# Kernel tuning notes

Hardware: AMD Instinct MI355X
Metric: run time of the kernel (lower is better)

The kernel has to match this reference:

```python
import jax, jax.numpy as jnp
import numpy as np

DIM = 256
FFN_DIM = 512
NH = 8
EPS = 1e-5


def ln(x, g, b):
    m = x.mean(-1, keepdims=True)
    v = ((x - m) ** 2).mean(-1, keepdims=True)
    return (x - m) / jnp.sqrt(v + EPS) * g + b


def setup_inputs() -> dict:
    key = jax.random.key(0)
    ks = jax.random.split(key, 16)
    B, L, C, H, W = 16, 16384, DIM, 128, 128
    s = 0.02
    return {
        "query": jax.random.normal(ks[0], (B, 1, C), jnp.float32),
        "mem": jax.random.normal(ks[1], (B, L, C), jnp.float32),
        "ior_emb": jax.random.uniform(ks[2], (B, NH, H, W), jnp.float32),
        # input_proj: Linear(dim,dim) + ReLU + LayerNorm
        "W_ip": jax.random.normal(ks[3], (C, C), jnp.float32) * s,
        "b_ip": jnp.zeros((C,), jnp.float32),
        "g_ip": jnp.ones((C,), jnp.float32),
        "be_ip": jnp.zeros((C,), jnp.float32),
        # q / kv projections
        "W_q": jax.random.normal(ks[4], (C, C), jnp.float32) * s,
        "b_q": jnp.zeros((C,), jnp.float32),
        "W_kv": jax.random.normal(ks[5], (C, 2 * C), jnp.float32) * s,
        "b_kv": jnp.zeros((2 * C,), jnp.float32),
        # norm_q, norm_ffn
        "g_q": jnp.ones((C,), jnp.float32),
        "be_q": jnp.zeros((C,), jnp.float32),
        "g_f": jnp.ones((C,), jnp.float32),
        "be_f": jnp.zeros((C,), jnp.float32),
        # ffn (Mlp)
        "W1": jax.random.normal(ks[6], (C, FFN_DIM), jnp.float32) * s,
        "b1": jnp.zeros((FFN_DIM,), jnp.float32),
        "W2": jax.random.normal(ks[7], (FFN_DIM, C), jnp.float32) * s,
        "b2": jnp.zeros((C,), jnp.float32),
    }


def reference(query, mem, ior_emb, W_ip, b_ip, g_ip, be_ip, W_q, b_q, W_kv, b_kv,
              g_q, be_q, g_f, be_f, W1, b1, W2, b2):
    B, L, C = mem.shape
    nh = ior_emb.shape[1]
    hd = C // nh
    scale = hd ** -0.5
    # input_proj(mem): Linear -> ReLU -> LayerNorm
    m = ln(jax.nn.relu(mem @ W_ip + b_ip), g_ip, be_ip)  # [B,L,C]
    kv = m @ W_kv + b_kv
    k, v = kv[..., :C], kv[..., C:]
    q = ln(query, g_q, be_q) @ W_q + b_q  # [B,1,C]
    # per-head split along channel == reshape (..., nh, hd)
    qh = q.reshape(B, 1, nh, hd)
    kh = k.reshape(B, L, nh, hd)
    vh = v.reshape(B, L, nh, hd)
    ior = ior_emb.reshape(B, nh, 1, L)
    scores = jnp.einsum('bqhd,blhd->bhql', qh, kh) * scale * ior  # [B,nh,1,L]
    attn = jax.nn.softmax(scores, axis=-1)
    out = jnp.einsum('bhql,blhd->bqhd', attn, vh).reshape(B, 1, C)
    x = out + query
    h = ln(x, g_f, be_f)
    ffn = jax.nn.gelu(h @ W1 + b1, approximate=False) @ W2 + b2
    return x + ffn
```

## Files before the change

kernel.cpp:

```cpp
#include <hip/hip_runtime.h>
#include <math.h>

#define CDIM 256
#define LDIM 16384
#define NH 8
#define HD 32
#define FFN 512
#define EPS 1e-5f
#define SCALE 0.17677669529663687f

#define RB 64
#define CHUNKS (LDIM/RB)
#define LDA 264

typedef __attribute__((ext_vector_type(8))) short short8;
typedef __attribute__((ext_vector_type(4))) float f32x4;

__device__ inline unsigned short f2bf(float x) {
    unsigned int u = __float_as_uint(x);
    unsigned int lsb = (u >> 16) & 1u;
    u += 0x7fffu + lsb;
    return (unsigned short)(u >> 16);
}


__global__ __launch_bounds__(256) void convert_weights(const float* __restrict__ Wip,
                                                       const float* __restrict__ Wkv,
                                                       unsigned short* __restrict__ w1,
                                                       unsigned short* __restrict__ wkv) {
    int idx = blockIdx.x * 256 + threadIdx.x;
    if (idx < 65536) {
        int j = idx & 7, l = (idx >> 3) & 63, c = (idx >> 9) & 15, t = idx >> 13;
        int k = t * 32 + (l >> 4) * 8 + j;
        int col = c * 16 + (l & 15);
        w1[idx] = f2bf(Wip[k * CDIM + col]);
    }
    if (idx < 131072) {
        int j = idx & 7, l = (idx >> 3) & 63, c = (idx >> 9) & 31, t = idx >> 14;
        int k = t * 32 + (l >> 4) * 8 + j;
        int col = c * 16 + (l & 15);
        wkv[idx] = f2bf(Wkv[k * 2 * CDIM + col]);
    }
}


__global__ __launch_bounds__(256) void qprep_kernel(const float* __restrict__ query,
                                                    const float* __restrict__ Wq,
                                                    const float* __restrict__ bq,
                                                    const float* __restrict__ gq,
                                                    const float* __restrict__ beq,
                                                    float* __restrict__ qs) {
    int b = blockIdx.x;
    int tid = threadIdx.x;
    int wave = tid >> 6, lane = tid & 63;
    __shared__ float sh[CDIM];
    __shared__ float red[8];

    float x = query[b * CDIM + tid];
    float s = x, sq = x * x;
#pragma unroll
    for (int m = 32; m >= 1; m >>= 1) { s += __shfl_xor(s, m, 64); sq += __shfl_xor(sq, m, 64); }
    if (lane == 0) { red[wave] = s; red[4 + wave] = sq; }
    __syncthreads();
    float ts = red[0] + red[1] + red[2] + red[3];
    float tq = red[4] + red[5] + red[6] + red[7];
    float mean = ts * (1.f / CDIM);
    float var = tq * (1.f / CDIM) - mean * mean;
    float rstd = rsqrtf(var + EPS);
    sh[tid] = (x - mean) * rstd * gq[tid] + beq[tid];
    __syncthreads();

    float acc = bq[tid];
    for (int k = 0; k < CDIM; ++k) acc = fmaf(sh[k], Wq[k * CDIM + tid], acc);
    qs[b * CDIM + tid] = acc * SCALE;
}


__device__ inline void mfma_gemm(const unsigned short* __restrict__ smA,
                                 const unsigned short* __restrict__ wsw, int NC, int ctile0,
                                 int lx, int quad, f32x4 acc[4][4]) {
#pragma unroll
    for (int rt = 0; rt < 4; ++rt)
#pragma unroll
        for (int ci = 0; ci < 4; ++ci) acc[rt][ci] = (f32x4){0.f, 0.f, 0.f, 0.f};

    int l = quad * 16 + lx;
#pragma unroll
    for (int t = 0; t < 8; ++t) {
        short8 bfrag[4];
#pragma unroll
        for (int ci = 0; ci < 4; ++ci)
            bfrag[ci] = *(const short8*)(wsw + (((size_t)(t * NC + ctile0 + ci)) * 64 + l) * 8);
        short8 afrag[4];
#pragma unroll
        for (int rt = 0; rt < 4; ++rt)
            afrag[rt] = *(const short8*)(smA + (rt * 16 + lx) * LDA + t * 32 + quad * 8);
#pragma unroll
        for (int rt = 0; rt < 4; ++rt)
#pragma unroll
            for (int ci = 0; ci < 4; ++ci)
                acc[rt][ci] = __builtin_amdgcn_mfma_f32_16x16x32_bf16(afrag[rt], bfrag[ci], acc[rt][ci], 0, 0, 0);
    }
}


__global__ __launch_bounds__(256, 2) void main_kernel(const float* __restrict__ mem,
                                                      const unsigned short* __restrict__ w1,
                                                      const unsigned short* __restrict__ wkv,
                                                      const float* __restrict__ bip,
                                                      const float* __restrict__ gip,
                                                      const float* __restrict__ beip,
                                                      const float* __restrict__ bkv,
                                                      const float* __restrict__ ior,
                                                      const float* __restrict__ qs,
                                                      float* __restrict__ partials) {
    int blk = blockIdx.x;
    int b = blk / CHUNKS;
    int chunk = blk % CHUNKS;
    int row0 = chunk * RB;
    int tid = threadIdx.x;
    int w = tid >> 6, l = tid & 63;
    int quad = l >> 4, lx = l & 15;

    __shared__ unsigned short bufA[RB * LDA];
    __shared__ float iorS[NH][RB];
    __shared__ float redS[4][RB];
    __shared__ float redQ[4][RB];
    __shared__ float stats[2][RB];

    {
        int i0 = tid, i1 = tid + 256;
        int h0 = i0 >> 6, r0 = i0 & 63;
        int h1 = i1 >> 6, r1 = i1 & 63;
        iorS[h0][r0] = ior[((size_t)(b * NH + h0)) * LDIM + row0 + r0];
        iorS[h1][r1] = ior[((size_t)(b * NH + h1)) * LDIM + row0 + r1];
    }
    {
        const float4* src = (const float4*)(mem + ((size_t)b * LDIM + row0) * CDIM);
#pragma unroll
        for (int it = 0; it < 16; ++it) {
            int i = tid + 256 * it;
            int r = i >> 6, c4 = i & 63;
            float4 v = src[i];
            ushort4 u;
            u.x = f2bf(v.x); u.y = f2bf(v.y); u.z = f2bf(v.z); u.w = f2bf(v.w);
            *(ushort4*)&bufA[r * LDA + c4 * 4] = u;
        }
    }
    __syncthreads();

    int col[4];
#pragma unroll
    for (int ci = 0; ci < 4; ++ci) col[ci] = (4 * w + ci) * 16 + lx;

    f32x4 acc[4][4];
    mfma_gemm(bufA, w1, 16, 4 * w, lx, quad, acc);

    float bb[4], gg[4], ee[4];
#pragma unroll
    for (int ci = 0; ci < 4; ++ci) { bb[ci] = bip[col[ci]]; gg[ci] = gip[col[ci]]; ee[ci] = beip[col[ci]]; }

#pragma unroll
    for (int rt = 0; rt < 4; ++rt) {
#pragma unroll
        for (int reg = 0; reg < 4; ++reg) {
#pragma unroll
            for (int ci = 0; ci < 4; ++ci)
                acc[rt][ci][reg] = fmaxf(acc[rt][ci][reg] + bb[ci], 0.f);
            float s = acc[rt][0][reg] + acc[rt][1][reg] + acc[rt][2][reg] + acc[rt][3][reg];
            float q = acc[rt][0][reg] * acc[rt][0][reg] + acc[rt][1][reg] * acc[rt][1][reg]
                    + acc[rt][2][reg] * acc[rt][2][reg] + acc[rt][3][reg] * acc[rt][3][reg];
#pragma unroll
            for (int m = 8; m >= 1; m >>= 1) { s += __shfl_xor(s, m, 64); q += __shfl_xor(q, m, 64); }
            if (lx == 0) {
                int row = rt * 16 + quad * 4 + reg;
                redS[w][row] = s;
                redQ[w][row] = q;
            }
        }
    }
    __syncthreads();
    if (tid < RB) {
        float s = redS[0][tid] + redS[1][tid] + redS[2][tid] + redS[3][tid];
        float q = redQ[0][tid] + redQ[1][tid] + redQ[2][tid] + redQ[3][tid];
        float mean = s * (1.f / CDIM);
        float var = q * (1.f / CDIM) - mean * mean;
        stats[0][tid] = mean;
        stats[1][tid] = rsqrtf(var + EPS);
    }
    __syncthreads();

#pragma unroll
    for (int rt = 0; rt < 4; ++rt)
#pragma unroll
        for (int reg = 0; reg < 4; ++reg) {
            int row = rt * 16 + quad * 4 + reg;
            float mean = stats[0][row], rstd = stats[1][row];
#pragma unroll
            for (int ci = 0; ci < 4; ++ci) {
                float y = (acc[rt][ci][reg] - mean) * rstd * gg[ci] + ee[ci];
                bufA[row * LDA + col[ci]] = f2bf(y);
            }
        }
    __syncthreads();

    f32x4 acc2[4][4];
    mfma_gemm(bufA, wkv, 32, 4 * w, lx, quad, acc2);

    float qv[4], bk[4];
#pragma unroll
    for (int ci = 0; ci < 4; ++ci) { qv[ci] = qs[b * CDIM + col[ci]]; bk[ci] = bkv[col[ci]]; }

    float p0[16], p1[16];
    float M0 = -1e30f, M1 = -1e30f;
#pragma unroll
    for (int rt = 0; rt < 4; ++rt)
#pragma unroll
        for (int reg = 0; reg < 4; ++reg) {
            float s0 = (acc2[rt][0][reg] + bk[0]) * qv[0] + (acc2[rt][1][reg] + bk[1]) * qv[1];
            float s1 = (acc2[rt][2][reg] + bk[2]) * qv[2] + (acc2[rt][3][reg] + bk[3]) * qv[3];
#pragma unroll
            for (int m = 8; m >= 1; m >>= 1) { s0 += __shfl_xor(s0, m, 64); s1 += __shfl_xor(s1, m, 64); }
            int row = rt * 16 + quad * 4 + reg;
            s0 *= iorS[2 * w][row];
            s1 *= iorS[2 * w + 1][row];
            p0[rt * 4 + reg] = s0;
            p1[rt * 4 + reg] = s1;
            M0 = fmaxf(M0, s0);
            M1 = fmaxf(M1, s1);
        }
    M0 = fmaxf(M0, __shfl_xor(M0, 16, 64)); M0 = fmaxf(M0, __shfl_xor(M0, 32, 64));
    M1 = fmaxf(M1, __shfl_xor(M1, 16, 64)); M1 = fmaxf(M1, __shfl_xor(M1, 32, 64));
    float S0 = 0.f, S1 = 0.f;
#pragma unroll
    for (int i = 0; i < 16; ++i) {
        p0[i] = __expf(p0[i] - M0); S0 += p0[i];
        p1[i] = __expf(p1[i] - M1); S1 += p1[i];
    }
    S0 += __shfl_xor(S0, 16, 64); S0 += __shfl_xor(S0, 32, 64);
    S1 += __shfl_xor(S1, 16, 64); S1 += __shfl_xor(S1, 32, 64);

    f32x4 acc3[4][4];
    mfma_gemm(bufA, wkv, 32, 16 + 4 * w, lx, quad, acc3);

    float o[4];
#pragma unroll
    for (int ci = 0; ci < 4; ++ci) {
        float bo = bkv[CDIM + col[ci]];
        const float* pp = (ci < 2) ? p0 : p1;
        float a = 0.f;
#pragma unroll
        for (int rt = 0; rt < 4; ++rt)
#pragma unroll
            for (int reg = 0; reg < 4; ++reg)
                a = fmaf(pp[rt * 4 + reg], acc3[rt][ci][reg] + bo, a);
        a += __shfl_xor(a, 16, 64);
        a += __shfl_xor(a, 32, 64);
        o[ci] = a;
    }

    float* P0 = &partials[((size_t)blk * NH + 2 * w) * 34];
    float* P1 = P0 + 34;
    if (quad == 0) {
        P0[2 + lx] = o[0];
        P0[2 + 16 + lx] = o[1];
        P1[2 + lx] = o[2];
        P1[2 + 16 + lx] = o[3];
        if (lx == 0) { P0[0] = M0; P0[1] = S0; P1[0] = M1; P1[1] = S1; }
    }
}


__global__ __launch_bounds__(64) void combine_kernel(const float* __restrict__ partials,
                                                     float* __restrict__ attnout) {
    int bh = blockIdx.x;
    int b = bh >> 3, h = bh & 7;
    int lane = threadIdx.x;

    float M = -1e30f;
    for (int c = lane; c < CHUNKS; c += 64)
        M = fmaxf(M, partials[(((size_t)b * CHUNKS + c) * NH + h) * 34]);
#pragma unroll
    for (int m = 32; m >= 1; m >>= 1) M = fmaxf(M, __shfl_xor(M, m, 64));

    float S = 0.f;
    for (int c = lane; c < CHUNKS; c += 64) {
        const float* P = &partials[(((size_t)b * CHUNKS + c) * NH + h) * 34];
        S += P[1] * __expf(P[0] - M);
    }
#pragma unroll
    for (int m = 32; m >= 1; m >>= 1) S += __shfl_xor(S, m, 64);

    int d = lane & 31, half = lane >> 5;
    float O = 0.f;
    for (int c = half; c < CHUNKS; c += 2) {
        const float* P = &partials[(((size_t)b * CHUNKS + c) * NH + h) * 34];
        O = fmaf(P[2 + d], __expf(P[0] - M), O);
    }
    O += __shfl_xor(O, 32, 64);
    if (lane < 32) attnout[b * CDIM + h * HD + d] = O / S;
}


__global__ __launch_bounds__(256) void epilogue_kernel(const float* __restrict__ attnout,
                                                       const float* __restrict__ query,
                                                       const float* __restrict__ gf,
                                                       const float* __restrict__ bef,
                                                       const float* __restrict__ W1,
                                                       const float* __restrict__ b1,
                                                       const float* __restrict__ W2,
                                                       const float* __restrict__ b2,
                                                       float* __restrict__ out) {
    int b = blockIdx.x;
    int tid = threadIdx.x;
    int wave = tid >> 6, lane = tid & 63;
    __shared__ float sh[FFN];
    __shared__ float red[8];

    float x = attnout[b * CDIM + tid] + query[b * CDIM + tid];
    float s = x, sq = x * x;
#pragma unroll
    for (int m = 32; m >= 1; m >>= 1) { s += __shfl_xor(s, m, 64); sq += __shfl_xor(sq, m, 64); }
    if (lane == 0) { red[wave] = s; red[4 + wave] = sq; }
    __syncthreads();
    float ts = red[0] + red[1] + red[2] + red[3];
    float tq = red[4] + red[5] + red[6] + red[7];
    float mean = ts * (1.f / CDIM);
    float var = tq * (1.f / CDIM) - mean * mean;
    float rstd = rsqrtf(var + EPS);
    sh[tid] = (x - mean) * rstd * gf[tid] + bef[tid];
    __syncthreads();

    float t[2];
#pragma unroll
    for (int i = 0; i < 2; ++i) {
        int f = tid + 256 * i;
        float a = b1[f];
        for (int k = 0; k < CDIM; ++k) a = fmaf(sh[k], W1[k * FFN + f], a);
        t[i] = 0.5f * a * (1.f + erff(a * 0.7071067811865476f));
    }
    __syncthreads();
    sh[tid] = t[0];
    sh[tid + 256] = t[1];
    __syncthreads();

    float y = b2[tid];
    for (int f = 0; f < FFN; ++f) y = fmaf(sh[f], W2[f * CDIM + tid], y);
    out[b * CDIM + tid] = x + y;
}


extern "C" void kernel_launch(void* const* d_in, const int* in_sizes, int n_in,
                              void* d_out, int out_size, void* d_ws, size_t ws_size,
                              hipStream_t stream) {
    const float* query = (const float*)d_in[0];
    const float* mem   = (const float*)d_in[1];
    const float* ior   = (const float*)d_in[2];
    const float* Wip   = (const float*)d_in[3];
    const float* bip   = (const float*)d_in[4];
    const float* gip   = (const float*)d_in[5];
    const float* beip  = (const float*)d_in[6];
    const float* Wq    = (const float*)d_in[7];
    const float* bq    = (const float*)d_in[8];
    const float* Wkv   = (const float*)d_in[9];
    const float* bkv   = (const float*)d_in[10];
    const float* gq    = (const float*)d_in[11];
    const float* beq   = (const float*)d_in[12];
    const float* gf    = (const float*)d_in[13];
    const float* bef   = (const float*)d_in[14];
    const float* W1    = (const float*)d_in[15];
    const float* b1    = (const float*)d_in[16];
    const float* W2    = (const float*)d_in[17];
    const float* b2    = (const float*)d_in[18];
    float* out = (float*)d_out;

    char* ws = (char*)d_ws;
    float* qs             = (float*)(ws);
    float* attnout        = (float*)(ws + 16384);
    float* partials       = (float*)(ws + 32768);
    unsigned short* w1sw  = (unsigned short*)(ws + 32768 + 4456448);
    unsigned short* wkvsw = (unsigned short*)(ws + 32768 + 4456448 + 131072);

    const int B = 16;

    convert_weights<<<512, 256, 0, stream>>>(Wip, Wkv, w1sw, wkvsw);
    qprep_kernel<<<B, 256, 0, stream>>>(query, Wq, bq, gq, beq, qs);
    main_kernel<<<B * CHUNKS, 256, 0, stream>>>(mem, w1sw, wkvsw, bip, gip, beip, bkv, ior, qs, partials);
    combine_kernel<<<B * NH, 64, 0, stream>>>(partials, attnout);
    epilogue_kernel<<<B, 256, 0, stream>>>(attnout, query, gf, bef, W1, b1, W2, b2, out);
}
```

Before: 612.8 us.

## Fold K and V projections into query-side and post-softmax matmuls

```diff
diff --git a/kernel.cpp b/kernel.cpp
--- a/kernel.cpp
+++ b/kernel.cpp
@@ -10,11 +10,14 @@
 #define SCALE 0.17677669529663687f
 
 #define RB 64
-#define CHUNKS (LDIM/RB)
+#define NCHUNK 256
 #define LDA 264
+#define PSTRIDE 258
 
 typedef __attribute__((ext_vector_type(8))) short short8;
 typedef __attribute__((ext_vector_type(4))) float f32x4;
+
+union U8 { short8 s8; unsigned u[4]; };
 
 __device__ inline unsigned short f2bf(float x) {
     unsigned int u = __float_as_uint(x);
@@ -25,22 +28,12 @@
 
 
 __global__ __launch_bounds__(256) void convert_weights(const float* __restrict__ Wip,
-                                                       const float* __restrict__ Wkv,
-                                                       unsigned short* __restrict__ w1,
-                                                       unsigned short* __restrict__ wkv) {
+                                                       unsigned short* __restrict__ w1) {
     int idx = blockIdx.x * 256 + threadIdx.x;
-    if (idx < 65536) {
-        int j = idx & 7, l = (idx >> 3) & 63, c = (idx >> 9) & 15, t = idx >> 13;
-        int k = t * 32 + (l >> 4) * 8 + j;
-        int col = c * 16 + (l & 15);
-        w1[idx] = f2bf(Wip[k * CDIM + col]);
-    }
-    if (idx < 131072) {
-        int j = idx & 7, l = (idx >> 3) & 63, c = (idx >> 9) & 31, t = idx >> 14;
-        int k = t * 32 + (l >> 4) * 8 + j;
-        int col = c * 16 + (l & 15);
-        wkv[idx] = f2bf(Wkv[k * 2 * CDIM + col]);
-    }
+    int j = idx & 7, l = (idx >> 3) & 63, c = (idx >> 9) & 15, t = idx >> 13;
+    int k = t * 32 + (l >> 4) * 8 + j;
+    int colc = c * 16 + (l & 15);
+    w1[idx] = f2bf(Wip[k * CDIM + colc]);
 }
 
 
@@ -49,11 +42,16 @@
                                                     const float* __restrict__ bq,
                                                     const float* __restrict__ gq,
                                                     const float* __restrict__ beq,
-                                                    float* __restrict__ qs) {
+                                                    const float* __restrict__ Wkv,
+                                                    const float* __restrict__ bkv,
+                                                    float* __restrict__ qs,
+                                                    unsigned short* __restrict__ wts,
+                                                    float* __restrict__ qcb) {
     int b = blockIdx.x;
     int tid = threadIdx.x;
     int wave = tid >> 6, lane = tid & 63;
     __shared__ float sh[CDIM];
+    __shared__ float qsh[CDIM];
     __shared__ float red[8];
 
     float x = query[b * CDIM + tid];
@@ -72,7 +70,34 @@
 
     float acc = bq[tid];
     for (int k = 0; k < CDIM; ++k) acc = fmaf(sh[k], Wq[k * CDIM + tid], acc);
-    qs[b * CDIM + tid] = acc * SCALE;
+    float qv = acc * SCALE;
+    qs[b * CDIM + tid] = qv;
+    qsh[tid] = qv;
+    __syncthreads();
+
+    float wa[8];
+#pragma unroll
+    for (int h = 0; h < 8; ++h) wa[h] = 0.f;
+    const float* wr = Wkv + (size_t)tid * (2 * CDIM);
+#pragma unroll
+    for (int h = 0; h < 8; ++h)
+#pragma unroll
+        for (int d = 0; d < 32; ++d)
+            wa[h] = fmaf(wr[h * 32 + d], qsh[h * 32 + d], wa[h]);
+    unsigned short* wb = wts + (b << 12) + ((tid >> 5) << 9) + (((tid >> 3) & 3) << 7) + (tid & 7);
+#pragma unroll
+    for (int h = 0; h < 8; ++h) wb[h << 3] = f2bf(wa[h]);
+#pragma unroll
+    for (int h = 8; h < 16; ++h) wb[h << 3] = 0;
+
+    if (tid < 16) {
+        float cb = 0.f;
+        if (tid < 8) {
+#pragma unroll
+            for (int d = 0; d < 32; ++d) cb = fmaf(bkv[tid * 32 + d], qsh[tid * 32 + d], cb);
+        }
+        qcb[b * 16 + tid] = cb;
+    }
 }
 
 
@@ -104,36 +129,53 @@
 }
 
 
-__global__ __launch_bounds__(256, 2) void main_kernel(const float* __restrict__ mem,
+__device__ inline void mfma_svec(const unsigned short* __restrict__ smA,
+                                 const unsigned short* __restrict__ wt,
+                                 int lx, int quad, f32x4 accS[4]) {
+#pragma unroll
+    for (int rt = 0; rt < 4; ++rt) accS[rt] = (f32x4){0.f, 0.f, 0.f, 0.f};
+    int l = quad * 16 + lx;
+#pragma unroll
+    for (int t = 0; t < 8; ++t) {
+        short8 bf = *(const short8*)(wt + ((t * 64 + l) << 3));
+        short8 af[4];
+#pragma unroll
+        for (int rt = 0; rt < 4; ++rt)
+            af[rt] = *(const short8*)(smA + (rt * 16 + lx) * LDA + t * 32 + quad * 8);
+#pragma unroll
+        for (int rt = 0; rt < 4; ++rt)
+            accS[rt] = __builtin_amdgcn_mfma_f32_16x16x32_bf16(af[rt], bf, accS[rt], 0, 0, 0);
+    }
+}
+
+
+__global__ __launch_bounds__(256, 4) void main_kernel(const float* __restrict__ mem,
                                                       const unsigned short* __restrict__ w1,
-                                                      const unsigned short* __restrict__ wkv,
+                                                      const unsigned short* __restrict__ wts,
                                                       const float* __restrict__ bip,
                                                       const float* __restrict__ gip,
                                                       const float* __restrict__ beip,
-                                                      const float* __restrict__ bkv,
+                                                      const float* __restrict__ qcb,
                                                       const float* __restrict__ ior,
-                                                      const float* __restrict__ qs,
                                                       float* __restrict__ partials) {
     int blk = blockIdx.x;
-    int b = blk / CHUNKS;
-    int chunk = blk % CHUNKS;
+    int b = blk >> 8;
+    int chunk = blk & 255;
     int row0 = chunk * RB;
     int tid = threadIdx.x;
-    int w = tid >> 6, l = tid & 63;
-    int quad = l >> 4, lx = l & 15;
+    int w = tid >> 6, lane = tid & 63;
+    int quad = lane >> 4, lx = lane & 15;
 
     __shared__ unsigned short bufA[RB * LDA];
-    __shared__ float iorS[NH][RB];
+    __shared__ float iorS[NH][66];
     __shared__ float redS[4][RB];
     __shared__ float redQ[4][RB];
     __shared__ float stats[2][RB];
 
     {
         int i0 = tid, i1 = tid + 256;
-        int h0 = i0 >> 6, r0 = i0 & 63;
-        int h1 = i1 >> 6, r1 = i1 & 63;
-        iorS[h0][r0] = ior[((size_t)(b * NH + h0)) * LDIM + row0 + r0];
-        iorS[h1][r1] = ior[((size_t)(b * NH + h1)) * LDIM + row0 + r1];
+        iorS[i0 >> 6][i0 & 63] = ior[((size_t)(b * NH + (i0 >> 6))) * LDIM + row0 + (i0 & 63)];
+        iorS[i1 >> 6][i1 & 63] = ior[((size_t)(b * NH + (i1 >> 6))) * LDIM + row0 + (i1 & 63)];
     }
     {
         const float4* src = (const float4*)(mem + ((size_t)b * LDIM + row0) * CDIM);
@@ -167,138 +209,182 @@
 #pragma unroll
             for (int ci = 0; ci < 4; ++ci)
                 acc[rt][ci][reg] = fmaxf(acc[rt][ci][reg] + bb[ci], 0.f);
-            float s = acc[rt][0][reg] + acc[rt][1][reg] + acc[rt][2][reg] + acc[rt][3][reg];
-            float q = acc[rt][0][reg] * acc[rt][0][reg] + acc[rt][1][reg] * acc[rt][1][reg]
-                    + acc[rt][2][reg] * acc[rt][2][reg] + acc[rt][3][reg] * acc[rt][3][reg];
-#pragma unroll
-            for (int m = 8; m >= 1; m >>= 1) { s += __shfl_xor(s, m, 64); q += __shfl_xor(q, m, 64); }
+            float s2 = acc[rt][0][reg] + acc[rt][1][reg] + acc[rt][2][reg] + acc[rt][3][reg];
+            float q2 = acc[rt][0][reg] * acc[rt][0][reg] + acc[rt][1][reg] * acc[rt][1][reg]
+                     + acc[rt][2][reg] * acc[rt][2][reg] + acc[rt][3][reg] * acc[rt][3][reg];
+#pragma unroll
+            for (int m = 8; m >= 1; m >>= 1) { s2 += __shfl_xor(s2, m, 64); q2 += __shfl_xor(q2, m, 64); }
             if (lx == 0) {
                 int row = rt * 16 + quad * 4 + reg;
-                redS[w][row] = s;
-                redQ[w][row] = q;
+                redS[w][row] = s2;
+                redQ[w][row] = q2;
             }
         }
     }
     __syncthreads();
     if (tid < RB) {
-        float s = redS[0][tid] + redS[1][tid] + redS[2][tid] + redS[3][tid];
-        float q = redQ[0][tid] + redQ[1][tid] + redQ[2][tid] + redQ[3][tid];
-        float mean = s * (1.f / CDIM);
-        float var = q * (1.f / CDIM) - mean * mean;
+        float s2 = redS[0][tid] + redS[1][tid] + redS[2][tid] + redS[3][tid];
+        float q2 = redQ[0][tid] + redQ[1][tid] + redQ[2][tid] + redQ[3][tid];
+        float mean = s2 * (1.f / CDIM);
+        float var = q2 * (1.f / CDIM) - mean * mean;
         stats[0][tid] = mean;
         stats[1][tid] = rsqrtf(var + EPS);
     }
     __syncthreads();
 
-#pragma unroll
-    for (int rt = 0; rt < 4; ++rt)
+    unsigned ypk0[4][4], ypk1[4][4];
+#pragma unroll
+    for (int rt = 0; rt < 4; ++rt) {
+        float mn[4], rs[4];
 #pragma unroll
         for (int reg = 0; reg < 4; ++reg) {
             int row = rt * 16 + quad * 4 + reg;
-            float mean = stats[0][row], rstd = stats[1][row];
-#pragma unroll
-            for (int ci = 0; ci < 4; ++ci) {
-                float y = (acc[rt][ci][reg] - mean) * rstd * gg[ci] + ee[ci];
-                bufA[row * LDA + col[ci]] = f2bf(y);
-            }
-        }
-    __syncthreads();
-
-    f32x4 acc2[4][4];
-    mfma_gemm(bufA, wkv, 32, 4 * w, lx, quad, acc2);
-
-    float qv[4], bk[4];
-#pragma unroll
-    for (int ci = 0; ci < 4; ++ci) { qv[ci] = qs[b * CDIM + col[ci]]; bk[ci] = bkv[col[ci]]; }
-
-    float p0[16], p1[16];
-    float M0 = -1e30f, M1 = -1e30f;
+            mn[reg] = stats[0][row];
+            rs[reg] = stats[1][row];
+        }
+#pragma unroll
+        for (int ci = 0; ci < 4; ++ci) {
+            unsigned short u0 = f2bf((acc[rt][ci][0] - mn[0]) * rs[0] * gg[ci] + ee[ci]);
+            unsigned short u1 = f2bf((acc[rt][ci][1] - mn[1]) * rs[1] * gg[ci] + ee[ci]);
+            unsigned short u2 = f2bf((acc[rt][ci][2] - mn[2]) * rs[2] * gg[ci] + ee[ci]);
+            unsigned short u3 = f2bf((acc[rt][ci][3] - mn[3]) * rs[3] * gg[ci] + ee[ci]);
+            int rbase = rt * 16 + quad * 4;
+            bufA[(rbase + 0) * LDA + col[ci]] = u0;
+            bufA[(rbase + 1) * LDA + col[ci]] = u1;
+            bufA[(rbase + 2) * LDA + col[ci]] = u2;
+            bufA[(rbase + 3) * LDA + col[ci]] = u3;
+            ypk0[rt][ci] = (unsigned)u0 | ((unsigned)u1 << 16);
+            ypk1[rt][ci] = (unsigned)u2 | ((unsigned)u3 << 16);
+        }
+    }
+    __syncthreads();
+
+    f32x4 accS[4];
+    mfma_svec(bufA, wts + ((size_t)b << 12), lx, quad, accS);
+
+    float qcv = qcb[(b << 4) + lx];
+    float p[16];
+    float cmax = -1e30f;
 #pragma unroll
     for (int rt = 0; rt < 4; ++rt)
 #pragma unroll
         for (int reg = 0; reg < 4; ++reg) {
-            float s0 = (acc2[rt][0][reg] + bk[0]) * qv[0] + (acc2[rt][1][reg] + bk[1]) * qv[1];
-            float s1 = (acc2[rt][2][reg] + bk[2]) * qv[2] + (acc2[rt][3][reg] + bk[3]) * qv[3];
-#pragma unroll
-            for (int m = 8; m >= 1; m >>= 1) { s0 += __shfl_xor(s0, m, 64); s1 += __shfl_xor(s1, m, 64); }
             int row = rt * 16 + quad * 4 + reg;
-            s0 *= iorS[2 * w][row];
-            s1 *= iorS[2 * w + 1][row];
-            p0[rt * 4 + reg] = s0;
-            p1[rt * 4 + reg] = s1;
-            M0 = fmaxf(M0, s0);
-            M1 = fmaxf(M1, s1);
-        }
-    M0 = fmaxf(M0, __shfl_xor(M0, 16, 64)); M0 = fmaxf(M0, __shfl_xor(M0, 32, 64));
-    M1 = fmaxf(M1, __shfl_xor(M1, 16, 64)); M1 = fmaxf(M1, __shfl_xor(M1, 32, 64));
-    float S0 = 0.f, S1 = 0.f;
-#pragma unroll
-    for (int i = 0; i < 16; ++i) {
-        p0[i] = __expf(p0[i] - M0); S0 += p0[i];
-        p1[i] = __expf(p1[i] - M1); S1 += p1[i];
-    }
-    S0 += __shfl_xor(S0, 16, 64); S0 += __shfl_xor(S0, 32, 64);
-    S1 += __shfl_xor(S1, 16, 64); S1 += __shfl_xor(S1, 32, 64);
-
-    f32x4 acc3[4][4];
-    mfma_gemm(bufA, wkv, 32, 16 + 4 * w, lx, quad, acc3);
-
-    float o[4];
-#pragma unroll
-    for (int ci = 0; ci < 4; ++ci) {
-        float bo = bkv[CDIM + col[ci]];
-        const float* pp = (ci < 2) ? p0 : p1;
-        float a = 0.f;
-#pragma unroll
-        for (int rt = 0; rt < 4; ++rt)
-#pragma unroll
-            for (int reg = 0; reg < 4; ++reg)
-                a = fmaf(pp[rt * 4 + reg], acc3[rt][ci][reg] + bo, a);
-        a += __shfl_xor(a, 16, 64);
-        a += __shfl_xor(a, 32, 64);
-        o[ci] = a;
-    }
-
-    float* P0 = &partials[((size_t)blk * NH + 2 * w) * 34];
-    float* P1 = P0 + 34;
-    if (quad == 0) {
-        P0[2 + lx] = o[0];
-        P0[2 + 16 + lx] = o[1];
-        P1[2 + lx] = o[2];
-        P1[2 + 16 + lx] = o[3];
-        if (lx == 0) { P0[0] = M0; P0[1] = S0; P1[0] = M1; P1[1] = S1; }
-    }
-}
-
-
-__global__ __launch_bounds__(64) void combine_kernel(const float* __restrict__ partials,
-                                                     float* __restrict__ attnout) {
+            float sc = (accS[rt][reg] + qcv) * iorS[lx & 7][row];
+            p[rt * 4 + reg] = sc;
+            cmax = fmaxf(cmax, sc);
+        }
+    cmax = fmaxf(cmax, __shfl_xor(cmax, 16, 64));
+    cmax = fmaxf(cmax, __shfl_xor(cmax, 32, 64));
+    float csum = 0.f;
+#pragma unroll
+    for (int i = 0; i < 16; ++i) { p[i] = __expf(p[i] - cmax); csum += p[i]; }
+    csum += __shfl_xor(csum, 16, 64);
+    csum += __shfl_xor(csum, 32, 64);
+
+    f32x4 accPV[4];
+#pragma unroll
+    for (int ci = 0; ci < 4; ++ci) accPV[ci] = (f32x4){0.f, 0.f, 0.f, 0.f};
+
+    int srcA = ((quad & 1) << 5) + lx;
+    int srcB = srcA + 16;
+    bool hiQ = quad >= 2;
+#pragma unroll
+    for (int t2 = 0; t2 < 2; ++t2) {
+        float pe[8];
+#pragma unroll
+        for (int jj = 0; jj < 4; ++jj) {
+            float v0 = __shfl(p[t2 * 8 + jj], srcA, 64);
+            float v1 = __shfl(p[t2 * 8 + 4 + jj], srcA, 64);
+            pe[jj] = hiQ ? v1 : v0;
+            float v2 = __shfl(p[t2 * 8 + jj], srcB, 64);
+            float v3 = __shfl(p[t2 * 8 + 4 + jj], srcB, 64);
+            pe[4 + jj] = hiQ ? v3 : v2;
+        }
+        U8 pa;
+        pa.u[0] = (unsigned)f2bf(pe[0]) | ((unsigned)f2bf(pe[1]) << 16);
+        pa.u[1] = (unsigned)f2bf(pe[2]) | ((unsigned)f2bf(pe[3]) << 16);
+        pa.u[2] = (unsigned)f2bf(pe[4]) | ((unsigned)f2bf(pe[5]) << 16);
+        pa.u[3] = (unsigned)f2bf(pe[6]) | ((unsigned)f2bf(pe[7]) << 16);
+
+#pragma unroll
+        for (int ci = 0; ci < 4; ++ci) {
+            unsigned a0 = (unsigned)__shfl((int)ypk0[t2 * 2][ci], srcA, 64);
+            unsigned b0 = (unsigned)__shfl((int)ypk0[t2 * 2 + 1][ci], srcA, 64);
+            unsigned a1 = (unsigned)__shfl((int)ypk1[t2 * 2][ci], srcA, 64);
+            unsigned b1 = (unsigned)__shfl((int)ypk1[t2 * 2 + 1][ci], srcA, 64);
+            unsigned a2 = (unsigned)__shfl((int)ypk0[t2 * 2][ci], srcB, 64);
+            unsigned b2 = (unsigned)__shfl((int)ypk0[t2 * 2 + 1][ci], srcB, 64);
+            unsigned a3 = (unsigned)__shfl((int)ypk1[t2 * 2][ci], srcB, 64);
+            unsigned b3 = (unsigned)__shfl((int)ypk1[t2 * 2 + 1][ci], srcB, 64);
+            U8 ub;
+            ub.u[0] = hiQ ? b0 : a0;
+            ub.u[1] = hiQ ? b1 : a1;
+            ub.u[2] = hiQ ? b2 : a2;
+            ub.u[3] = hiQ ? b3 : a3;
+            accPV[ci] = __builtin_amdgcn_mfma_f32_16x16x32_bf16(pa.s8, ub.s8, accPV[ci], 0, 0, 0);
+        }
+    }
+
+    size_t pb = ((size_t)(b * NCHUNK + chunk)) * NH * PSTRIDE;
+    if (quad < 2) {
+#pragma unroll
+        for (int reg = 0; reg < 4; ++reg) {
+            float* dst = partials + pb + (size_t)(quad * 4 + reg) * PSTRIDE;
+#pragma unroll
+            for (int ci = 0; ci < 4; ++ci) dst[col[ci]] = accPV[ci][reg];
+        }
+    }
+    if (quad == 0 && lx < 8) {
+        float* dst = partials + pb + (size_t)lx * PSTRIDE;
+        dst[256] = cmax;
+        dst[257] = csum;
+    }
+}
+
+
+__global__ __launch_bounds__(256) void combine_kernel(const float* __restrict__ partials,
+                                                      const float* __restrict__ Wkv,
+                                                      const float* __restrict__ bkv,
+                                                      float* __restrict__ attnout) {
     int bh = blockIdx.x;
     int b = bh >> 3, h = bh & 7;
-    int lane = threadIdx.x;
-
+    int tid = threadIdx.x;
+    __shared__ float ms[NCHUNK], wf[NCHUNK], mt[CDIM];
+    __shared__ float sredA[4];
+    __shared__ float ored[8][33];
+
+    const float* base = partials + ((size_t)b * NCHUNK * NH + h) * PSTRIDE;
+    ms[tid] = base[(size_t)tid * NH * PSTRIDE + 256];
+    __syncthreads();
     float M = -1e30f;
-    for (int c = lane; c < CHUNKS; c += 64)
-        M = fmaxf(M, partials[(((size_t)b * CHUNKS + c) * NH + h) * 34]);
-#pragma unroll
-    for (int m = 32; m >= 1; m >>= 1) M = fmaxf(M, __shfl_xor(M, m, 64));
-
-    float S = 0.f;
-    for (int c = lane; c < CHUNKS; c += 64) {
-        const float* P = &partials[(((size_t)b * CHUNKS + c) * NH + h) * 34];
-        S += P[1] * __expf(P[0] - M);
-    }
-#pragma unroll
-    for (int m = 32; m >= 1; m >>= 1) S += __shfl_xor(S, m, 64);
-
-    int d = lane & 31, half = lane >> 5;
-    float O = 0.f;
-    for (int c = half; c < CHUNKS; c += 2) {
-        const float* P = &partials[(((size_t)b * CHUNKS + c) * NH + h) * 34];
-        O = fmaf(P[2 + d], __expf(P[0] - M), O);
-    }
-    O += __shfl_xor(O, 32, 64);
-    if (lane < 32) attnout[b * CDIM + h * HD + d] = O / S;
+    for (int s = 0; s < NCHUNK; ++s) M = fmaxf(M, ms[s]);
+    float e = __expf(ms[tid] - M);
+    wf[tid] = e;
+    float Sl = base[(size_t)tid * NH * PSTRIDE + 257] * e;
+#pragma unroll
+    for (int m = 32; m >= 1; m >>= 1) Sl += __shfl_xor(Sl, m, 64);
+    if ((tid & 63) == 0) sredA[tid >> 6] = Sl;
+    __syncthreads();
+    float St = sredA[0] + sredA[1] + sredA[2] + sredA[3];
+
+    float acc = 0.f;
+    for (int s = 0; s < NCHUNK; ++s) acc = fmaf(wf[s], base[(size_t)s * NH * PSTRIDE + tid], acc);
+    mt[tid] = acc / St;
+    __syncthreads();
+
+    int d = tid & 31, g = tid >> 5;
+    float a2 = 0.f;
+    for (int c = g * 32; c < g * 32 + 32; ++c)
+        a2 = fmaf(mt[c], Wkv[(size_t)c * (2 * CDIM) + CDIM + h * 32 + d], a2);
+    ored[g][d] = a2;
+    __syncthreads();
+    if (tid < 32) {
+        float o = bkv[CDIM + h * 32 + tid];
+#pragma unroll
+        for (int gg2 = 0; gg2 < 8; ++gg2) o += ored[gg2][tid];
+        attnout[b * CDIM + h * HD + tid] = o;
+    }
 }
 
 
@@ -377,15 +463,16 @@
     char* ws = (char*)d_ws;
     float* qs             = (float*)(ws);
     float* attnout        = (float*)(ws + 16384);
-    float* partials       = (float*)(ws + 32768);
-    unsigned short* w1sw  = (unsigned short*)(ws + 32768 + 4456448);
-    unsigned short* wkvsw = (unsigned short*)(ws + 32768 + 4456448 + 131072);
+    float* qcb            = (float*)(ws + 32768);
+    unsigned short* w1sw  = (unsigned short*)(ws + 33792);
+    unsigned short* wtsw  = (unsigned short*)(ws + 164864);
+    float* partials       = (float*)(ws + 295936);
 
     const int B = 16;
 
-    convert_weights<<<512, 256, 0, stream>>>(Wip, Wkv, w1sw, wkvsw);
-    qprep_kernel<<<B, 256, 0, stream>>>(query, Wq, bq, gq, beq, qs);
-    main_kernel<<<B * CHUNKS, 256, 0, stream>>>(mem, w1sw, wkvsw, bip, gip, beip, bkv, ior, qs, partials);
-    combine_kernel<<<B * NH, 64, 0, stream>>>(partials, attnout);
+    convert_weights<<<256, 256, 0, stream>>>(Wip, w1sw);
+    qprep_kernel<<<B, 256, 0, stream>>>(query, Wq, bq, gq, beq, Wkv, bkv, qs, wtsw, qcb);
+    main_kernel<<<B * NCHUNK, 256, 0, stream>>>(mem, w1sw, wtsw, bip, gip, beip, qcb, ior, partials);
+    combine_kernel<<<B * NH, 256, 0, stream>>>(partials, Wkv, bkv, attnout);
     epilogue_kernel<<<B, 256, 0, stream>>>(attnout, query, gf, bef, W1, b1, W2, b2, out);
 }
```

Result: faster. 526.5 us (-14.1%).
